# Kernel tuning notes

Measured on AMD Instinct MI355X. Metric: run time of the kernel, lower is better.

## Reference

```python
import jax, jax.numpy as jnp
import numpy as np

HEADS = 8
DIM_HEAD = 64
SCALE = DIM_HEAD ** -0.5


def setup_inputs() -> dict:
    key = jax.random.key(0)
    ks = jax.random.split(key, 7)
    b, n, m = 2, 4096, 4096
    query_dim, context_dim, inner = 1024, 768, HEADS * DIM_HEAD
    s = 0.02
    return {
        "x": jax.random.normal(ks[0], (b, n, query_dim), jnp.float32),
        "context": jax.random.normal(ks[1], (b, m, context_dim), jnp.float32),
        "Wq": jax.random.normal(ks[2], (query_dim, inner), jnp.float32) * s,
        "Wk": jax.random.normal(ks[3], (context_dim, inner), jnp.float32) * s,
        "Wv": jax.random.normal(ks[4], (context_dim, inner), jnp.float32) * s,
        "Wo": jax.random.normal(ks[5], (inner, query_dim), jnp.float32) * s,
        "bo": jnp.zeros((query_dim,), jnp.float32),
    }


def reference(x, context, Wq, Wk, Wv, Wo, bo):
    b, n, _ = x.shape
    m = context.shape[1]
    # projections (no bias), split heads: b n (h d) -> b n h d
    q = (x @ Wq).reshape(b, n, HEADS, DIM_HEAD)
    k = (context @ Wk).reshape(b, m, HEADS, DIM_HEAD)
    v = (context @ Wv).reshape(b, m, HEADS, DIM_HEAD)
    # fp32 QK^T (ATTN_PRECISION='fp32' path), full [b,h,n,m] scores
    sim = jnp.einsum("bihd,bjhd->bhij", q.astype(jnp.float32), k.astype(jnp.float32)) * SCALE
    attn = jax.nn.softmax(sim, axis=-1).astype(v.dtype)
    out = jnp.einsum("bhij,bjhd->bihd", attn, v).reshape(b, n, HEADS * DIM_HEAD)
    # to_out: Linear with bias (dropout=0 is identity)
    return out @ Wo + bo
```

## Files before the change

kernel.cpp:

```cpp
#include <hip/hip_runtime.h>
#include <hip/hip_bf16.h>
#include <cmath>


using bf16_t = __hip_bfloat16;
typedef __bf16 bf16x8 __attribute__((ext_vector_type(8)));
typedef float  f32x4  __attribute__((ext_vector_type(4)));

static constexpr int BATCH = 2;
static constexpr int NQ    = 4096;
static constexpr int NKV   = 4096;
static constexpr int NH    = 8;
static constexpr int DH    = 64;
static constexpr int INNER = NH * DH;
static constexpr int QDIM  = 1024;
static constexpr int CDIM  = 768;
static constexpr float QSCALE = 0.125f * 1.4426950408889634f;

#define MFMA_BF16(a, b, c) __builtin_amdgcn_mfma_f32_16x16x32_bf16((a), (b), (c), 0, 0, 0)

__device__ __forceinline__ float fast_exp2(float x) {
  return __builtin_amdgcn_exp2f(x);
}

__device__ __forceinline__ void gload16(const bf16_t* g, bf16_t* l) {
  __builtin_amdgcn_global_load_lds((__attribute__((address_space(1))) void*)(g),
                                   (__attribute__((address_space(3))) void*)(l),
                                   16, 0, 0);
}

__global__ __launch_bounds__(256) void cast2_kernel(const float* __restrict__ x,
                                                    bf16_t* __restrict__ xb, int xn8,
                                                    const float* __restrict__ c,
                                                    bf16_t* __restrict__ cb, int cn8) {
  int id = blockIdx.x * 256 + threadIdx.x;
  const float* in;
  bf16_t* out;
  if (id < xn8) {
    in = x; out = xb;
  } else {
    id -= xn8;
    if (id >= cn8) return;
    in = c; out = cb;
  }
  float4 a = ((const float4*)in)[2 * id];
  float4 b = ((const float4*)in)[2 * id + 1];
  bf16_t t[8] = {__float2bfloat16(a.x), __float2bfloat16(a.y), __float2bfloat16(a.z),
                 __float2bfloat16(a.w), __float2bfloat16(b.x), __float2bfloat16(b.y),
                 __float2bfloat16(b.z), __float2bfloat16(b.w)};
  ((uint4*)out)[id] = *(const uint4*)t;
}

__global__ __launch_bounds__(256) void wtrans4_kernel(const float* __restrict__ Wq,
                                                      const float* __restrict__ Wk,
                                                      const float* __restrict__ Wv,
                                                      const float* __restrict__ Wo,
                                                      bf16_t* __restrict__ WqT,
                                                      bf16_t* __restrict__ WkvT,
                                                      bf16_t* __restrict__ WoT) {
  __shared__ float tile[32][33];
  const float* W;
  bf16_t* WT;
  int K, N;
  switch (blockIdx.z) {
    case 0: W = Wq; WT = WqT; K = QDIM; N = INNER; break;
    case 1: W = Wk; WT = WkvT; K = CDIM; N = INNER; break;
    case 2: W = Wv; WT = WkvT + (size_t)INNER * CDIM; K = CDIM; N = INNER; break;
    default: W = Wo; WT = WoT; K = INNER; N = QDIM; break;
  }
  const int bn = blockIdx.x * 32, bk = blockIdx.y * 32;
  if (bn >= N || bk >= K) return;
  const int tx = threadIdx.x & 31, ty = threadIdx.x >> 5;
  for (int yy = ty; yy < 32; yy += 8)
    tile[yy][tx] = W[(size_t)(bk + yy) * N + bn + tx];
  __syncthreads();
  for (int yy = ty; yy < 32; yy += 8)
    WT[(size_t)(bn + yy) * K + bk + tx] = __float2bfloat16(tile[tx][yy]);
}

template <int OUT_MODE>
__global__ __launch_bounds__(256) void gemm_kernel(const bf16_t* __restrict__ A,
                                                   const bf16_t* __restrict__ WT,
                                                   void* __restrict__ Cp,
                                                   void* __restrict__ Cp2,
                                                   const float* __restrict__ bias,
                                                   float ascale, int M, int N, int K) {
  __shared__ __align__(16) bf16_t As[2][128][32];
  __shared__ __align__(16) bf16_t Bs[2][128][32];
  const int tid = threadIdx.x;
  const int lane = tid & 63, wave = tid >> 6;
  const int lane15 = lane & 15, quad = lane >> 4;
  const int wm = (wave >> 1) * 64, wn = (wave & 1) * 64;
  const int m0 = blockIdx.x * 128, n0 = blockIdx.y * 128;

  const f32x4 vzero = {0.f, 0.f, 0.f, 0.f};
  f32x4 acc[4][4];
  for (int i = 0; i < 4; ++i)
    for (int j = 0; j < 4; ++j) acc[i][j] = vzero;

  const int srow = tid >> 2, sc8 = (tid & 3) * 8;
  const bf16_t* aptr = A + (size_t)(m0 + srow) * K + sc8;
  const bf16_t* bptr = WT + (size_t)(n0 + srow) * K + sc8;
  bf16_t* const abase = &As[0][wave * 16][0];
  bf16_t* const bbase = &Bs[0][wave * 16][0];
  const int bufstride = 128 * 32;

  auto stage = [&](int t, int cur) {
    const bf16_t* as = aptr + t * 32;
    const bf16_t* bs = bptr + t * 32;
    bf16_t* ab = abase + cur * bufstride;
    bf16_t* bb = bbase + cur * bufstride;
    gload16(as, ab);
    gload16(as + (size_t)64 * K, ab + 64 * 32);
    gload16(bs, bb);
    gload16(bs + (size_t)64 * K, bb + 64 * 32);
  };

  const int T = K / 32;
  stage(0, 0);
  for (int t = 0; t < T; ++t) {
    const int cur = t & 1;
    __syncthreads();
    if (t + 1 < T) stage(t + 1, cur ^ 1);
    bf16x8 af[4], bfr[4];
    for (int i = 0; i < 4; ++i)
      af[i] = *reinterpret_cast<const bf16x8*>(&As[cur][wm + i * 16 + lane15][quad * 8]);
    for (int j = 0; j < 4; ++j)
      bfr[j] = *reinterpret_cast<const bf16x8*>(&Bs[cur][wn + j * 16 + lane15][quad * 8]);
    for (int i = 0; i < 4; ++i)
      for (int j = 0; j < 4; ++j) acc[i][j] = MFMA_BF16(af[i], bfr[j], acc[i][j]);
  }

  for (int i = 0; i < 4; ++i) {
    int gm = m0 + wm + i * 16 + quad * 4;
    for (int j = 0; j < 4; ++j) {
      int gn = n0 + wn + j * 16 + lane15;
      for (int r = 0; r < 4; ++r) {
        float v = acc[i][j][r];
        if constexpr (OUT_MODE == 0) {
          ((bf16_t*)Cp)[(size_t)(gm + r) * N + gn] = __float2bfloat16(v * ascale);
        } else if constexpr (OUT_MODE == 1) {
          ((float*)Cp)[(size_t)(gm + r) * N + gn] = v + bias[gn];
        } else {
          if (gn < INNER) {
            ((bf16_t*)Cp)[(size_t)(gm + r) * INNER + gn] = __float2bfloat16(v);
          } else {
            int gmr = gm + r;
            ((bf16_t*)Cp2)[((size_t)(gmr >> 12) * INNER + (gn - INNER)) * (size_t)NKV +
                           (gmr & 4095)] = __float2bfloat16(v);
          }
        }
      }
    }
  }
}

__global__ __launch_bounds__(512) void attn_kernel(const bf16_t* Qg ,
                                                   const bf16_t* __restrict__ Kg ,
                                                   const bf16_t* __restrict__ Vtg ,
                                                   bf16_t* Og ) {
  __shared__ __align__(16) bf16_t KsF[2][8][512];
  __shared__ __align__(16) bf16_t VtF[2][8][512];
  __shared__ __align__(16) bf16_t PsA[128][72];

  const int tid = threadIdx.x;
  const int lane = tid & 63, wave = tid >> 6;
  const int lane15 = lane & 15, quad = lane >> 4;
  const int wrow = wave * 16;
  const int q0 = blockIdx.x * 128;
  const int h = blockIdx.y;
  const int b = blockIdx.z;

  const size_t qbase  = ((size_t)b * NQ + q0) * INNER + h * DH;
  const size_t kbase  = ((size_t)b * NKV) * INNER + h * DH;
  const size_t vtbase = ((size_t)(b * NH + h) * DH) * NKV;

  bf16x8 qf[2];
  for (int ks = 0; ks < 2; ++ks)
    qf[ks] = *reinterpret_cast<const bf16x8*>(
        Qg + qbase + (size_t)(wrow + lane15) * INNER + ks * 32 + quad * 8);

  bf16x8 ones;
  for (int i = 0; i < 8; ++i) ones[i] = (__bf16)1.0f;

  const f32x4 vzero = {0.f, 0.f, 0.f, 0.f};
  f32x4 acc_o[4];
  f32x4 acc_l = vzero;
  for (int j = 0; j < 4; ++j) acc_o[j] = vzero;

  const int cw = wave;
  auto kaddr = [&](int kv0) {
    return Kg + kbase + (size_t)(kv0 + (cw & 3) * 16 + lane15) * INNER + (cw >> 2) * 32 + quad * 8;
  };
  auto vaddr = [&](int kv0) {
    return Vtg + vtbase + (size_t)((cw & 3) * 16 + lane15) * NKV + kv0 + (cw >> 2) * 32 + quad * 8;
  };
  uint4 kr = *(const uint4*)kaddr(0);
  uint4 vr = *(const uint4*)vaddr(0);

  constexpr int T = NKV / 64;
  for (int t = 0; t < T; ++t) {
    const int cur = t & 1;
    *(uint4*)&KsF[cur][cw][lane * 8] = kr;
    *(uint4*)&VtF[cur][cw][lane * 8] = vr;
    __syncthreads();

    f32x4 acc_st[4];
    for (int j = 0; j < 4; ++j) acc_st[j] = vzero;
    for (int ks = 0; ks < 2; ++ks) {
      bf16x8 kf[4];
      for (int j = 0; j < 4; ++j)
        kf[j] = *reinterpret_cast<const bf16x8*>(&KsF[cur][ks * 4 + j][lane * 8]);
      for (int j = 0; j < 4; ++j) acc_st[j] = MFMA_BF16(kf[j], qf[ks], acc_st[j]);
    }

    if (t + 1 < T) {
      int kv0n = (t + 1) * 64;
      kr = *(const uint4*)kaddr(kv0n);
      vr = *(const uint4*)vaddr(kv0n);
    }

    for (int j = 0; j < 4; ++j) {
      bf16_t t4[4];
      for (int r = 0; r < 4; ++r)
        t4[r] = __float2bfloat16(fast_exp2(acc_st[j][r]));
      *(uint2*)&PsA[wrow + lane15][j * 16 + quad * 4] = *(const uint2*)t4;
    }
    asm volatile("s_waitcnt lgkmcnt(0)" ::: "memory");

    for (int ks = 0; ks < 2; ++ks) {
      bf16x8 pf, vf[4];
      pf = *reinterpret_cast<const bf16x8*>(&PsA[wrow + lane15][ks * 32 + quad * 8]);
      for (int j = 0; j < 4; ++j)
        vf[j] = *reinterpret_cast<const bf16x8*>(&VtF[cur][ks * 4 + j][lane * 8]);
      acc_l = MFMA_BF16(pf, ones, acc_l);
      for (int j = 0; j < 4; ++j) acc_o[j] = MFMA_BF16(pf, vf[j], acc_o[j]);
    }
  }

  for (int r = 0; r < 4; ++r) {
    float invr = 1.f / acc_l[r];
    int row = wrow + quad * 4 + r;
    for (int j = 0; j < 4; ++j)
      Og[qbase + (size_t)row * INNER + j * 16 + lane15] =
          __float2bfloat16(acc_o[j][r] * invr);
  }
}

extern "C" void kernel_launch(void* const* d_in, const int* in_sizes, int n_in,
                              void* d_out, int out_size, void* d_ws, size_t ws_size,
                              hipStream_t stream) {
  (void)in_sizes; (void)n_in; (void)out_size; (void)ws_size;
  const float* x   = (const float*)d_in[0];
  const float* ctx = (const float*)d_in[1];
  const float* Wq  = (const float*)d_in[2];
  const float* Wk  = (const float*)d_in[3];
  const float* Wv  = (const float*)d_in[4];
  const float* Wo  = (const float*)d_in[5];
  const float* bo  = (const float*)d_in[6];
  float* out = (float*)d_out;

  char* ws = (char*)d_ws;
  size_t off = 0;
  auto take = [&](size_t nelem) { bf16_t* p = (bf16_t*)(ws + off); off += nelem * 2; return p; };
  bf16_t* WqT  = take((size_t)INNER * QDIM);
  bf16_t* WkvT = take((size_t)(2 * INNER) * CDIM);
  bf16_t* WoT  = take((size_t)QDIM * INNER);
  bf16_t* qob  = take((size_t)BATCH * NQ * INNER);
  bf16_t* kb   = take((size_t)BATCH * NKV * INNER);
  bf16_t* vtb  = take((size_t)BATCH * INNER * NKV);

  bf16_t* xb   = (bf16_t*)d_out;
  bf16_t* ctxb = xb + (size_t)BATCH * NQ * QDIM;

  const int M = BATCH * NQ;
  const int xN8 = BATCH * NQ * QDIM / 8, cN8 = BATCH * NKV * CDIM / 8;

  cast2_kernel<<<(xN8 + cN8 + 255) / 256, 256, 0, stream>>>(x, xb, xN8, ctx, ctxb, cN8);
  wtrans4_kernel<<<dim3(32, 32, 4), 256, 0, stream>>>(Wq, Wk, Wv, Wo, WqT, WkvT, WoT);

  gemm_kernel<0><<<dim3(M / 128, INNER / 128), 256, 0, stream>>>(
      xb, WqT, qob, nullptr, nullptr, QSCALE, M, INNER, QDIM);
  gemm_kernel<3><<<dim3(M / 128, (2 * INNER) / 128), 256, 0, stream>>>(
      ctxb, WkvT, kb, vtb, nullptr, 1.f, M, 2 * INNER, CDIM);

  attn_kernel<<<dim3(NQ / 128, NH, BATCH), 512, 0, stream>>>(qob, kb, vtb, qob);

  gemm_kernel<1><<<dim3(M / 128, QDIM / 128), 256, 0, stream>>>(
      qob, WoT, out, nullptr, bo, 1.f, M, QDIM, INNER);
}
```

Before: 264.8 us.

## Merge Q and KV projection GEMMs, shrink GEMM M-tile, prioritize attention MFMAs

Replaces the templated GEMM with a shared 64x128-tile core, merges the Q and KV projection GEMMs into one launch, and uses the smaller tile for the output projection too. The smaller tile doubles block count to improve CU occupancy on the modest-sized GEMMs and removes one kernel launch. Separately it wraps the attention MFMA loops in s_setprio to favour matrix issue over other waves. Smaller tiles lower A-tile reuse and add redundant B loads per output.

Result: no change. 262.7 us (-0.8%).

```diff
diff --git a/kernel.cpp b/kernel.cpp
--- a/kernel.cpp
+++ b/kernel.cpp
@@ -78,42 +78,28 @@
     WT[(size_t)(bn + yy) * K + bk + tx] = __float2bfloat16(tile[tx][yy]);
 }
 
-template <int OUT_MODE>
-__global__ __launch_bounds__(256) void gemm_kernel(const bf16_t* __restrict__ A,
-                                                   const bf16_t* __restrict__ WT,
-                                                   void* __restrict__ Cp,
-                                                   void* __restrict__ Cp2,
-                                                   const float* __restrict__ bias,
-                                                   float ascale, int M, int N, int K) {
-  __shared__ __align__(16) bf16_t As[2][128][32];
-  __shared__ __align__(16) bf16_t Bs[2][128][32];
-  const int tid = threadIdx.x;
+__device__ __forceinline__ void gemm64_core(const bf16_t* __restrict__ A,
+                                            const bf16_t* __restrict__ WT, int K,
+                                            int m0, int n0, int tid,
+                                            f32x4 (&acc)[2][4],
+                                            bf16_t (*As)[64][32],
+                                            bf16_t (*Bs)[128][32]) {
   const int lane = tid & 63, wave = tid >> 6;
   const int lane15 = lane & 15, quad = lane >> 4;
-  const int wm = (wave >> 1) * 64, wn = (wave & 1) * 64;
-  const int m0 = blockIdx.x * 128, n0 = blockIdx.y * 128;
-
-  const f32x4 vzero = {0.f, 0.f, 0.f, 0.f};
-  f32x4 acc[4][4];
-  for (int i = 0; i < 4; ++i)
-    for (int j = 0; j < 4; ++j) acc[i][j] = vzero;
-
+  const int wm = (wave >> 1) * 32, wn = (wave & 1) * 64;
   const int srow = tid >> 2, sc8 = (tid & 3) * 8;
   const bf16_t* aptr = A + (size_t)(m0 + srow) * K + sc8;
   const bf16_t* bptr = WT + (size_t)(n0 + srow) * K + sc8;
   bf16_t* const abase = &As[0][wave * 16][0];
   bf16_t* const bbase = &Bs[0][wave * 16][0];
-  const int bufstride = 128 * 32;
+  constexpr int ABUF = 64 * 32, BBUF = 128 * 32;
 
   auto stage = [&](int t, int cur) {
     const bf16_t* as = aptr + t * 32;
     const bf16_t* bs = bptr + t * 32;
-    bf16_t* ab = abase + cur * bufstride;
-    bf16_t* bb = bbase + cur * bufstride;
-    gload16(as, ab);
-    gload16(as + (size_t)64 * K, ab + 64 * 32);
-    gload16(bs, bb);
-    gload16(bs + (size_t)64 * K, bb + 64 * 32);
+    gload16(as, abase + cur * ABUF);
+    gload16(bs, bbase + cur * BBUF);
+    gload16(bs + (size_t)64 * K, bbase + cur * BBUF + 64 * 32);
   };
 
   const int T = K / 32;
@@ -122,35 +108,89 @@
     const int cur = t & 1;
     __syncthreads();
     if (t + 1 < T) stage(t + 1, cur ^ 1);
-    bf16x8 af[4], bfr[4];
-    for (int i = 0; i < 4; ++i)
+    bf16x8 af[2], bfr[4];
+    for (int i = 0; i < 2; ++i)
       af[i] = *reinterpret_cast<const bf16x8*>(&As[cur][wm + i * 16 + lane15][quad * 8]);
     for (int j = 0; j < 4; ++j)
       bfr[j] = *reinterpret_cast<const bf16x8*>(&Bs[cur][wn + j * 16 + lane15][quad * 8]);
-    for (int i = 0; i < 4; ++i)
+    for (int i = 0; i < 2; ++i)
       for (int j = 0; j < 4; ++j) acc[i][j] = MFMA_BF16(af[i], bfr[j], acc[i][j]);
   }
-
-  for (int i = 0; i < 4; ++i) {
+}
+
+__global__ __launch_bounds__(256) void qkv_gemm_kernel(const bf16_t* __restrict__ xb,
+                                                       const bf16_t* __restrict__ ctxb,
+                                                       const bf16_t* __restrict__ WqT,
+                                                       const bf16_t* __restrict__ WkvT,
+                                                       bf16_t* __restrict__ qob,
+                                                       bf16_t* __restrict__ kb,
+                                                       bf16_t* __restrict__ vtb) {
+  __shared__ __align__(16) bf16_t As[2][64][32];
+  __shared__ __align__(16) bf16_t Bs[2][128][32];
+  const int tid = threadIdx.x;
+  const bool isq = blockIdx.y < 4;
+  const bf16_t* A  = isq ? xb : ctxb;
+  const bf16_t* WT = isq ? WqT : WkvT;
+  const int K  = isq ? QDIM : CDIM;
+  const int m0 = blockIdx.x * 64;
+  const int n0 = (isq ? blockIdx.y : blockIdx.y - 4) * 128;
+
+  const f32x4 vzero = {0.f, 0.f, 0.f, 0.f};
+  f32x4 acc[2][4];
+  for (int i = 0; i < 2; ++i)
+    for (int j = 0; j < 4; ++j) acc[i][j] = vzero;
+
+  gemm64_core(A, WT, K, m0, n0, tid, acc, As, Bs);
+
+  const int lane = tid & 63, wave = tid >> 6;
+  const int lane15 = lane & 15, quad = lane >> 4;
+  const int wm = (wave >> 1) * 32, wn = (wave & 1) * 64;
+  for (int i = 0; i < 2; ++i) {
     int gm = m0 + wm + i * 16 + quad * 4;
     for (int j = 0; j < 4; ++j) {
       int gn = n0 + wn + j * 16 + lane15;
       for (int r = 0; r < 4; ++r) {
         float v = acc[i][j][r];
-        if constexpr (OUT_MODE == 0) {
-          ((bf16_t*)Cp)[(size_t)(gm + r) * N + gn] = __float2bfloat16(v * ascale);
-        } else if constexpr (OUT_MODE == 1) {
-          ((float*)Cp)[(size_t)(gm + r) * N + gn] = v + bias[gn];
+        if (isq) {
+          qob[(size_t)(gm + r) * INNER + gn] = __float2bfloat16(v * QSCALE);
+        } else if (gn < INNER) {
+          kb[(size_t)(gm + r) * INNER + gn] = __float2bfloat16(v);
         } else {
-          if (gn < INNER) {
-            ((bf16_t*)Cp)[(size_t)(gm + r) * INNER + gn] = __float2bfloat16(v);
-          } else {
-            int gmr = gm + r;
-            ((bf16_t*)Cp2)[((size_t)(gmr >> 12) * INNER + (gn - INNER)) * (size_t)NKV +
-                           (gmr & 4095)] = __float2bfloat16(v);
-          }
+          int gmr = gm + r;
+          vtb[((size_t)(gmr >> 12) * INNER + (gn - INNER)) * (size_t)NKV +
+              (gmr & 4095)] = __float2bfloat16(v);
         }
       }
+    }
+  }
+}
+
+__global__ __launch_bounds__(256) void out_gemm_kernel(const bf16_t* __restrict__ A,
+                                                       const bf16_t* __restrict__ WT,
+                                                       float* __restrict__ C,
+                                                       const float* __restrict__ bias) {
+  __shared__ __align__(16) bf16_t As[2][64][32];
+  __shared__ __align__(16) bf16_t Bs[2][128][32];
+  const int tid = threadIdx.x;
+  const int m0 = blockIdx.x * 64, n0 = blockIdx.y * 128;
+  constexpr int K = INNER, N = QDIM;
+
+  const f32x4 vzero = {0.f, 0.f, 0.f, 0.f};
+  f32x4 acc[2][4];
+  for (int i = 0; i < 2; ++i)
+    for (int j = 0; j < 4; ++j) acc[i][j] = vzero;
+
+  gemm64_core(A, WT, K, m0, n0, tid, acc, As, Bs);
+
+  const int lane = tid & 63, wave = tid >> 6;
+  const int lane15 = lane & 15, quad = lane >> 4;
+  const int wm = (wave >> 1) * 32, wn = (wave & 1) * 64;
+  for (int i = 0; i < 2; ++i) {
+    int gm = m0 + wm + i * 16 + quad * 4;
+    for (int j = 0; j < 4; ++j) {
+      int gn = n0 + wn + j * 16 + lane15;
+      for (int r = 0; r < 4; ++r)
+        C[(size_t)(gm + r) * N + gn] = acc[i][j][r] + bias[gn];
     }
   }
 }
@@ -207,12 +247,14 @@
 
     f32x4 acc_st[4];
     for (int j = 0; j < 4; ++j) acc_st[j] = vzero;
+    __builtin_amdgcn_s_setprio(1);
     for (int ks = 0; ks < 2; ++ks) {
       bf16x8 kf[4];
       for (int j = 0; j < 4; ++j)
         kf[j] = *reinterpret_cast<const bf16x8*>(&KsF[cur][ks * 4 + j][lane * 8]);
       for (int j = 0; j < 4; ++j) acc_st[j] = MFMA_BF16(kf[j], qf[ks], acc_st[j]);
     }
+    __builtin_amdgcn_s_setprio(0);
 
     if (t + 1 < T) {
       int kv0n = (t + 1) * 64;
@@ -228,6 +270,7 @@
     }
     asm volatile("s_waitcnt lgkmcnt(0)" ::: "memory");
 
+    __builtin_amdgcn_s_setprio(1);
     for (int ks = 0; ks < 2; ++ks) {
       bf16x8 pf, vf[4];
       pf = *reinterpret_cast<const bf16x8*>(&PsA[wrow + lane15][ks * 32 + quad * 8]);
@@ -236,6 +279,7 @@
       acc_l = MFMA_BF16(pf, ones, acc_l);
       for (int j = 0; j < 4; ++j) acc_o[j] = MFMA_BF16(pf, vf[j], acc_o[j]);
     }
+    __builtin_amdgcn_s_setprio(0);
   }
 
   for (int r = 0; r < 4; ++r) {
@@ -279,13 +323,9 @@
   cast2_kernel<<<(xN8 + cN8 + 255) / 256, 256, 0, stream>>>(x, xb, xN8, ctx, ctxb, cN8);
   wtrans4_kernel<<<dim3(32, 32, 4), 256, 0, stream>>>(Wq, Wk, Wv, Wo, WqT, WkvT, WoT);
 
-  gemm_kernel<0><<<dim3(M / 128, INNER / 128), 256, 0, stream>>>(
-      xb, WqT, qob, nullptr, nullptr, QSCALE, M, INNER, QDIM);
-  gemm_kernel<3><<<dim3(M / 128, (2 * INNER) / 128), 256, 0, stream>>>(
-      ctxb, WkvT, kb, vtb, nullptr, 1.f, M, 2 * INNER, CDIM);
+  qkv_gemm_kernel<<<dim3(M / 64, 12), 256, 0, stream>>>(xb, ctxb, WqT, WkvT, qob, kb, vtb);
 
   attn_kernel<<<dim3(NQ / 128, NH, BATCH), 512, 0, stream>>>(qob, kb, vtb, qob);
 
-  gemm_kernel<1><<<dim3(M / 128, QDIM / 128), 256, 0, stream>>>(
-      qob, WoT, out, nullptr, bo, 1.f, M, QDIM, INNER);
-}
+  out_gemm_kernel<<<dim3(M / 64, QDIM / 128), 256, 0, stream>>>(qob, WoT, out, bo);
+}
```
